# Optimization experiments

Measured on AMD Instinct MI355X. Metric: run time of the kernel, lower is better.

## Reference

```python
import jax, jax.numpy as jnp
import numpy as np

DIM = 512          # model dim
DH = 32            # dim_head
WSZ = 8            # window_size
HEADS = DIM // DH  # 16
INNER = HEADS * DH # 512
D4 = DIM // 4      # DPB hidden = 128
EPS = 1e-5


def _ln(x, g, b=None, eps=EPS):
    m = jnp.mean(x, axis=-1, keepdims=True)
    v = jnp.var(x, axis=-1, keepdims=True)
    y = (x - m) * jax.lax.rsqrt(v + eps) * g
    return y if b is None else y + b


def setup_inputs() -> dict:
    key = jax.random.key(0)
    ks = jax.random.split(key, 8)
    g = lambda k, shape, s=0.02: (jax.random.normal(k, shape, jnp.float32) * s)
    return {
        "x": jax.random.normal(ks[0], (16, 64, 64, DIM), jnp.float32),
        "norm_g": jnp.ones((DIM,), jnp.float32),
        "norm_b": jnp.zeros((DIM,), jnp.float32),
        "w_qkv": g(ks[1], (DIM, 3 * INNER)),
        "w_out": g(ks[2], (INNER, DIM)),
        "b_out": jnp.zeros((DIM,), jnp.float32),
        "dpb_w0": g(ks[3], (2, D4)), "dpb_b0": jnp.zeros((D4,), jnp.float32), "dpb_ln0": jnp.ones((D4,), jnp.float32),
        "dpb_w1": g(ks[4], (D4, D4)), "dpb_b1": jnp.zeros((D4,), jnp.float32), "dpb_ln1": jnp.ones((D4,), jnp.float32),
        "dpb_w2": g(ks[5], (D4, D4)), "dpb_b2": jnp.zeros((D4,), jnp.float32), "dpb_ln2": jnp.ones((D4,), jnp.float32),
        "dpb_w3": g(ks[6], (D4, 1)), "dpb_b3": jnp.zeros((1,), jnp.float32),
    }


def reference(x, norm_g, norm_b, w_qkv, w_out, b_out,
              dpb_w0, dpb_b0, dpb_ln0,
              dpb_w1, dpb_b1, dpb_ln1,
              dpb_w2, dpb_b2, dpb_ln2,
              dpb_w3, dpb_b3):
    B, H, W, d = x.shape
    w = WSZ
    scale = DH ** -0.5

    x = _ln(x, norm_g, norm_b)

    # 'short' attention: partition into non-overlapping wxw windows
    # b (h s1) (w s2) d -> (b h w) s1 s2 d
    xw = x.reshape(B, H // w, w, W // w, w, d).transpose(0, 1, 3, 2, 4, 5)
    xw = xw.reshape(-1, w, w, d)  # [nb, w, w, d]

    qkv = xw @ w_qkv  # 1x1 conv == dense, no bias
    q, k, v = jnp.split(qkv, 3, axis=-1)
    to_heads = lambda t: t.reshape(t.shape[0], w * w, HEADS, DH).transpose(0, 2, 1, 3)
    q, k, v = map(to_heads, (q, k, v))  # [nb, h, w*w, dh]

    sim = jnp.einsum('bhid,bhjd->bhij', q * scale, k)  # [nb, h, w*w, w*w]

    # relative-position gather indices (static)
    pos = jnp.arange(w)
    grid = jnp.stack(jnp.meshgrid(pos, pos, indexing='ij'), axis=-1).reshape(-1, 2)
    rel = grid[:, None] - grid[None, :] + (w - 1)
    rel_pos_indices = rel[..., 0] * (2 * w - 1) + rel[..., 1]  # [w*w, w*w]

    # dynamic position bias MLP over the (2w+1)^2 relative offsets
    p = jnp.arange(-w, w + 1)
    rp = jnp.stack(jnp.meshgrid(p, p, indexing='ij'), axis=-1).reshape(-1, 2).astype(jnp.float32)
    h = jax.nn.relu(_ln(rp @ dpb_w0 + dpb_b0, dpb_ln0))
    h = jax.nn.relu(_ln(h @ dpb_w1 + dpb_b1, dpb_ln1))
    h = jax.nn.relu(_ln(h @ dpb_w2 + dpb_b2, dpb_ln2))
    biases = (h @ dpb_w3 + dpb_b3)[:, 0]  # [(2w+1)^2]

    sim = sim + biases[rel_pos_indices]
    attn = jax.nn.softmax(sim, axis=-1)
    out = jnp.einsum('bhij,bhjd->bhid', attn, v)

    out = out.transpose(0, 2, 1, 3).reshape(-1, w, w, INNER)
    out = out @ w_out + b_out  # 1x1 conv with bias

    # (b h w) s1 s2 d -> b (h s1) (w s2) d
    out = out.reshape(B, H // w, W // w, w, w, d).transpose(0, 1, 3, 2, 4, 5)
    return out.reshape(B, H, W, d)
```

## Files before the change

### kernel.cpp

```cpp
#include <hip/hip_runtime.h>
#include <cstdint>
#include <cstddef>

typedef unsigned short u16;
typedef __attribute__((ext_vector_type(8))) short short8;
typedef __attribute__((ext_vector_type(4))) float f32x4;
typedef __attribute__((ext_vector_type(4))) unsigned short us4;

#define AS1 __attribute__((address_space(1)))
#define AS3 __attribute__((address_space(3)))

__device__ __forceinline__ u16 f2bf(float f) {
  union { float f; unsigned u; } v; v.f = f;
  unsigned r = v.u + 0x7fffu + ((v.u >> 16) & 1u);
  return (u16)(r >> 16);
}

__device__ __forceinline__ void gload_lds16(const u16* g, u16* l) {
  __builtin_amdgcn_global_load_lds((AS1 void*)g, (AS3 void*)l, 16, 0, 0);
}

__global__ void ln_cast_kernel(const float* __restrict__ x, const float* __restrict__ g,
                               const float* __restrict__ b, u16* __restrict__ out) {
  const int lane = threadIdx.x & 63;
  const int tok = blockIdx.x * 4 + (threadIdx.x >> 6);
  const float4* row = (const float4*)(x + (size_t)tok * 512);
  float4 v0 = row[lane];
  float4 v1 = row[lane + 64];
  float s = v0.x + v0.y + v0.z + v0.w + v1.x + v1.y + v1.z + v1.w;
  float q = v0.x*v0.x + v0.y*v0.y + v0.z*v0.z + v0.w*v0.w
          + v1.x*v1.x + v1.y*v1.y + v1.z*v1.z + v1.w*v1.w;
#pragma unroll
  for (int m = 1; m < 64; m <<= 1) { s += __shfl_xor(s, m, 64); q += __shfl_xor(q, m, 64); }
  const float mean = s * (1.0f / 512.0f);
  const float var = q * (1.0f / 512.0f) - mean * mean;
  const float r = rsqrtf(var + 1e-5f);
  const float4* g4 = (const float4*)g;
  const float4* b4 = (const float4*)b;
  float4 ga = g4[lane], gb = g4[lane + 64];
  float4 ba = b4[lane], bb = b4[lane + 64];
  us4 o0 = { f2bf((v0.x - mean) * r * ga.x + ba.x), f2bf((v0.y - mean) * r * ga.y + ba.y),
             f2bf((v0.z - mean) * r * ga.z + ba.z), f2bf((v0.w - mean) * r * ga.w + ba.w) };
  us4 o1 = { f2bf((v1.x - mean) * r * gb.x + bb.x), f2bf((v1.y - mean) * r * gb.y + bb.y),
             f2bf((v1.z - mean) * r * gb.z + bb.z), f2bf((v1.w - mean) * r * gb.w + bb.w) };
  *(us4*)(out + (size_t)tok * 512 + lane * 4) = o0;
  *(us4*)(out + (size_t)tok * 512 + 256 + lane * 4) = o1;
}

__global__ void prep_w_kernel(const float* __restrict__ wqkv, const float* __restrict__ wout,
                              u16* __restrict__ wqkvT, u16* __restrict__ woutT) {
  int idx = blockIdx.x * blockDim.x + threadIdx.x;
  if (idx < 512 * 1536) {
    int n = idx >> 9, k = idx & 511;
    wqkvT[idx] = f2bf(wqkv[k * 1536 + n]);
  } else {
    int j = idx - 512 * 1536;
    if (j < 512 * 512) {
      int n = j >> 9, k = j & 511;
      woutT[j] = f2bf(wout[k * 512 + n]);
    }
  }
}

__device__ __forceinline__ float lnrelu128(float a, float g, float* red, int tid) {
  float s = a, q = a * a;
#pragma unroll
  for (int m = 1; m < 64; m <<= 1) { s += __shfl_xor(s, m, 64); q += __shfl_xor(q, m, 64); }
  __syncthreads();
  if ((tid & 63) == 0) { red[tid >> 6] = s; red[2 + (tid >> 6)] = q; }
  __syncthreads();
  float S = red[0] + red[1], Q = red[2] + red[3];
  float mean = S * (1.f / 128.f);
  float var = Q * (1.f / 128.f) - mean * mean;
  float y = (a - mean) * rsqrtf(var + 1e-5f) * g;
  return fmaxf(y, 0.f);
}

__global__ void dpb_mlp_kernel(const float* __restrict__ w0, const float* __restrict__ b0, const float* __restrict__ g0,
                               const float* __restrict__ w1, const float* __restrict__ b1, const float* __restrict__ g1,
                               const float* __restrict__ w2, const float* __restrict__ b2, const float* __restrict__ g2,
                               const float* __restrict__ w3, const float* __restrict__ b3,
                               float* __restrict__ biases) {
  __shared__ float h[128];
  __shared__ float red[4];
  const int tid = threadIdx.x;
  const int row = blockIdx.x;
  const float p0 = (float)(row / 17) - 8.0f;
  const float p1 = (float)(row % 17) - 8.0f;
  float a = p0 * w0[tid] + p1 * w0[128 + tid] + b0[tid];
  a = lnrelu128(a, g0[tid], red, tid);
  h[tid] = a;
  __syncthreads();
  float acc = b1[tid];
  for (int i = 0; i < 128; ++i) acc += h[i] * w1[i * 128 + tid];
  acc = lnrelu128(acc, g1[tid], red, tid);
  h[tid] = acc;
  __syncthreads();
  float acc2 = b2[tid];
  for (int i = 0; i < 128; ++i) acc2 += h[i] * w2[i * 128 + tid];
  acc2 = lnrelu128(acc2, g2[tid], red, tid);
  float t = acc2 * w3[tid];
#pragma unroll
  for (int m = 1; m < 64; m <<= 1) t += __shfl_xor(t, m, 64);
  __syncthreads();
  if ((tid & 63) == 0) red[tid >> 6] = t;
  __syncthreads();
  if (tid == 0) biases[row] = red[0] + red[1] + b3[0];
}

__global__ void dpb_table_kernel(const float* __restrict__ biases, float* __restrict__ table) {
  int t = blockIdx.x * blockDim.x + threadIdx.x;
  if (t < 4096) {
    int i = t >> 6, j = t & 63;
    int r0 = (i >> 3) - (j >> 3) + 7;
    int r1 = (i & 7) - (j & 7) + 7;
    table[t] = biases[r0 * 15 + r1];
  }
}

template <int CT, bool F32OUT>
__global__ __launch_bounds__(512, 2) void gemm256_kernel(const u16* __restrict__ A, const u16* __restrict__ BT,
                                                         void* __restrict__ Cv, const float* __restrict__ bias) {
  __shared__ __align__(16) u16 lds[65536];
  const int tid = threadIdx.x;
  const int w = tid >> 6, l = tid & 63;
  const int wm = w >> 2, wn = w & 3;
  const int cr = l & 15, cg = l >> 4;
  const int pc8 = (cg ^ ((cr + (cr >> 2)) & 3)) * 8;

  const int hw = blockIdx.x;
  const int ix = hw >> 3;
  const int rt = (hw & 7) + 8 * (ix / CT);
  const int ct = ix % CT;
  const size_t brow = (size_t)rt * 256;
  const size_t bcol = (size_t)ct * 256;
  const int N = CT * 256;

  const int srow = tid >> 2;
  const int sch8 = ((tid & 3) ^ ((srow + (srow >> 2)) & 3)) * 8;

  const f32x4 zero = {0.f, 0.f, 0.f, 0.f};
  f32x4 acc[8][4];
#pragma unroll
  for (int i = 0; i < 8; ++i)
#pragma unroll
    for (int j = 0; j < 4; ++j) acc[i][j] = zero;

  const u16* aP = &lds[(wm * 128 + cr) * 32 + pc8];
  const u16* bP = &lds[(wn * 64 + cr) * 32 + pc8];

#define STAGE_HALF(G, GROW0, KCOL, LBASE)                                          \
  do {                                                                             \
    const u16* g0_ = (G) + ((GROW0) + srow) * 512 + (KCOL) + sch8;                 \
    gload_lds16(g0_, &lds[(LBASE) + w * 512]);                                     \
    gload_lds16(g0_ + 128 * 512, &lds[(LBASE) + 4096 + w * 512]);                  \
  } while (0)

  STAGE_HALF(A, brow, 0, 0);
  STAGE_HALF(BT, bcol, 0, 32768);
  STAGE_HALF(A, brow, 32, 8192);
  STAGE_HALF(BT, bcol, 32, 32768 + 8192);
  asm volatile("s_waitcnt vmcnt(4)" ::: "memory");
  __builtin_amdgcn_s_barrier();
  __builtin_amdgcn_sched_barrier(0);

#pragma unroll 2
  for (int kt = 0; kt < 8; ++kt) {
    const int cur = kt & 1;
    const int nbuf = cur ^ 1;
    const int ktn = (kt < 7) ? kt + 1 : 7;
    const int kcn = ktn * 64;
    const int abase = cur * 16384;
    const int bbase = 32768 + cur * 16384;
    short8 af[8], bfr[4];

#pragma unroll
    for (int fr = 0; fr < 8; ++fr) af[fr] = *(const short8*)(aP + abase + fr * 512);
#pragma unroll
    for (int c = 0; c < 4; ++c) bfr[c] = *(const short8*)(bP + bbase + c * 512);
    STAGE_HALF(A, brow, kcn, nbuf * 16384);
    STAGE_HALF(BT, bcol, kcn, 32768 + nbuf * 16384);
    asm volatile("s_waitcnt lgkmcnt(0)" ::: "memory");
    __builtin_amdgcn_sched_barrier(0);
    __builtin_amdgcn_s_setprio(1);
#pragma unroll
    for (int fr = 0; fr < 8; ++fr)
#pragma unroll
      for (int fc = 0; fc < 4; ++fc)
        acc[fr][fc] = __builtin_amdgcn_mfma_f32_16x16x32_bf16(bfr[fc], af[fr], acc[fr][fc], 0, 0, 0);
    __builtin_amdgcn_s_setprio(0);
    asm volatile("s_waitcnt vmcnt(4)" ::: "memory");
    __builtin_amdgcn_s_barrier();
    __builtin_amdgcn_sched_barrier(0);

#pragma unroll
    for (int fr = 0; fr < 8; ++fr) af[fr] = *(const short8*)(aP + abase + 8192 + fr * 512);
#pragma unroll
    for (int c = 0; c < 4; ++c) bfr[c] = *(const short8*)(bP + bbase + 8192 + c * 512);
    STAGE_HALF(A, brow, kcn + 32, nbuf * 16384 + 8192);
    STAGE_HALF(BT, bcol, kcn + 32, 32768 + nbuf * 16384 + 8192);
    asm volatile("s_waitcnt lgkmcnt(0)" ::: "memory");
    __builtin_amdgcn_sched_barrier(0);
    __builtin_amdgcn_s_setprio(1);
#pragma unroll
    for (int fr = 0; fr < 8; ++fr)
#pragma unroll
      for (int fc = 0; fc < 4; ++fc)
        acc[fr][fc] = __builtin_amdgcn_mfma_f32_16x16x32_bf16(bfr[fc], af[fr], acc[fr][fc], 0, 0, 0);
    __builtin_amdgcn_s_setprio(0);
    asm volatile("s_waitcnt vmcnt(4)" ::: "memory");
    __builtin_amdgcn_s_barrier();
    __builtin_amdgcn_sched_barrier(0);
  }
#undef STAGE_HALF

  asm volatile("s_waitcnt vmcnt(0)" ::: "memory");
  __builtin_amdgcn_sched_barrier(0);

  if (F32OUT) {
    float* C = (float*)Cv;
#pragma unroll
    for (int fc = 0; fc < 4; ++fc) {
      size_t col = bcol + wn * 64 + fc * 16 + cg * 4;
      float4 bv = *(const float4*)&bias[col];
#pragma unroll
      for (int fr = 0; fr < 8; ++fr) {
        size_t r = brow + wm * 128 + fr * 16 + cr;
        float4 o = { acc[fr][fc][0] + bv.x, acc[fr][fc][1] + bv.y,
                     acc[fr][fc][2] + bv.z, acc[fr][fc][3] + bv.w };
        *(float4*)(C + r * N + col) = o;
      }
    }
  } else {
    u16* C = (u16*)Cv;
#pragma unroll
    for (int fc = 0; fc < 4; ++fc) {
      size_t col = bcol + wn * 64 + fc * 16 + cg * 4;
#pragma unroll
      for (int fr = 0; fr < 8; ++fr) {
        size_t r = brow + wm * 128 + fr * 16 + cr;
        uint2 p;
        p.x = (unsigned)f2bf(acc[fr][fc][0]) | ((unsigned)f2bf(acc[fr][fc][1]) << 16);
        p.y = (unsigned)f2bf(acc[fr][fc][2]) | ((unsigned)f2bf(acc[fr][fc][3]) << 16);
        *(uint2*)(C + r * N + col) = p;
      }
    }
  }
}

__global__ __launch_bounds__(64) void attn_kernel(const u16* __restrict__ qkv,
                                                  const float* __restrict__ table,
                                                  u16* __restrict__ aout) {
  __shared__ __align__(16) u16 P[64 * 72];
  __shared__ __align__(16) u16 VT[32 * 72];
  const int l = threadIdx.x;
  const int cr = l & 15, cg = l >> 4;
  const int head = blockIdx.x & 15;
  const int win = blockIdx.x >> 4;
  const int base = ((win >> 6) << 12) + (((win >> 3) & 7) << 9) + ((win & 7) << 3);

  {
    const size_t row = base + ((l >> 3) << 6) + (l & 7);
    const u16* vp = qkv + row * 1536 + 1024 + head * 32;
    short8 v0 = *(const short8*)(vp);
    short8 v1 = *(const short8*)(vp + 8);
    short8 v2 = *(const short8*)(vp + 16);
    short8 v3 = *(const short8*)(vp + 24);
#pragma unroll
    for (int j = 0; j < 8; ++j) {
      VT[j * 72 + l] = (u16)v0[j];
      VT[(8 + j) * 72 + l] = (u16)v1[j];
      VT[(16 + j) * 72 + l] = (u16)v2[j];
      VT[(24 + j) * 72 + l] = (u16)v3[j];
    }
  }

  short8 qf[4], kf[4];
#pragma unroll
  for (int mt = 0; mt < 4; ++mt) {
    int t = mt * 16 + cr;
    size_t row = base + ((t >> 3) << 6) + (t & 7);
    qf[mt] = *(const short8*)(qkv + row * 1536 + head * 32 + cg * 8);
    kf[mt] = *(const short8*)(qkv + row * 1536 + 512 + head * 32 + cg * 8);
  }

  const f32x4 zero = {0.f, 0.f, 0.f, 0.f};
  f32x4 s[4][4];
#pragma unroll
  for (int mt = 0; mt < 4; ++mt)
#pragma unroll
    for (int nt = 0; nt < 4; ++nt)
      s[mt][nt] = __builtin_amdgcn_mfma_f32_16x16x32_bf16(qf[mt], kf[nt], zero, 0, 0, 0);

  const float scale = 0.17677669529663689f;
#pragma unroll
  for (int mt = 0; mt < 4; ++mt) {
#pragma unroll
    for (int reg = 0; reg < 4; ++reg) {
      const int r = mt * 16 + cg * 4 + reg;
      float v[4];
      float mx = -3.0e38f;
#pragma unroll
      for (int nt = 0; nt < 4; ++nt) {
        v[nt] = s[mt][nt][reg] * scale + table[r * 64 + nt * 16 + cr];
        mx = fmaxf(mx, v[nt]);
      }
#pragma unroll
      for (int m2 = 1; m2 < 16; m2 <<= 1) mx = fmaxf(mx, __shfl_xor(mx, m2, 64));
      float sum = 0.f;
#pragma unroll
      for (int nt = 0; nt < 4; ++nt) { v[nt] = __expf(v[nt] - mx); sum += v[nt]; }
#pragma unroll
      for (int m2 = 1; m2 < 16; m2 <<= 1) sum += __shfl_xor(sum, m2, 64);
      float inv = 1.0f / sum;
#pragma unroll
      for (int nt = 0; nt < 4; ++nt) P[r * 72 + nt * 16 + cr] = f2bf(v[nt] * inv);
    }
  }
  __syncthreads();

  f32x4 o[4][2];
#pragma unroll
  for (int mt = 0; mt < 4; ++mt) { o[mt][0] = zero; o[mt][1] = zero; }
#pragma unroll
  for (int kk = 0; kk < 2; ++kk) {
    short8 pf[4], vf[2];
#pragma unroll
    for (int mt = 0; mt < 4; ++mt) pf[mt] = *(const short8*)&P[(mt * 16 + cr) * 72 + kk * 32 + cg * 8];
#pragma unroll
    for (int n2 = 0; n2 < 2; ++n2) vf[n2] = *(const short8*)&VT[(n2 * 16 + cr) * 72 + kk * 32 + cg * 8];
#pragma unroll
    for (int mt = 0; mt < 4; ++mt)
#pragma unroll
      for (int n2 = 0; n2 < 2; ++n2)
        o[mt][n2] = __builtin_amdgcn_mfma_f32_16x16x32_bf16(pf[mt], vf[n2], o[mt][n2], 0, 0, 0);
  }

#pragma unroll
  for (int mt = 0; mt < 4; ++mt)
#pragma unroll
    for (int n2 = 0; n2 < 2; ++n2)
#pragma unroll
      for (int reg = 0; reg < 4; ++reg) {
        int t = mt * 16 + cg * 4 + reg;
        size_t row = base + ((t >> 3) << 6) + (t & 7);
        aout[row * 512 + head * 32 + n2 * 16 + cr] = f2bf(o[mt][n2][reg]);
      }
}

extern "C" void kernel_launch(void* const* d_in, const int* in_sizes, int n_in,
                              void* d_out, int out_size, void* d_ws, size_t ws_size,
                              hipStream_t stream) {
  const float* x = (const float*)d_in[0];
  const float* norm_g = (const float*)d_in[1];
  const float* norm_b = (const float*)d_in[2];
  const float* w_qkv = (const float*)d_in[3];
  const float* w_out = (const float*)d_in[4];
  const float* b_out = (const float*)d_in[5];
  const float* dw0 = (const float*)d_in[6];
  const float* db0 = (const float*)d_in[7];
  const float* dg0 = (const float*)d_in[8];
  const float* dw1 = (const float*)d_in[9];
  const float* db1 = (const float*)d_in[10];
  const float* dg1 = (const float*)d_in[11];
  const float* dw2 = (const float*)d_in[12];
  const float* db2 = (const float*)d_in[13];
  const float* dg2 = (const float*)d_in[14];
  const float* dw3 = (const float*)d_in[15];
  const float* db3 = (const float*)d_in[16];

  char* ws = (char*)d_ws;
  size_t off = 0;
  auto take = [&](size_t bytes) { char* p = ws + off; off += (bytes + 255) & ~(size_t)255; return p; };
  u16* xln = (u16*)take(65536ull * 512 * 2);
  u16* wqkvT = (u16*)take(1536 * 512 * 2);
  u16* woutT = (u16*)take(512 * 512 * 2);
  float* biases = (float*)take(289 * 4);
  float* table = (float*)take(4096 * 4);

  size_t rem = (ws_size > off) ? ws_size - off : 0;
  int nch = 4;
  if (rem >= 65536ull * 2048 * 2 + 512) nch = 1;
  else if (rem >= 32768ull * 2048 * 2 + 512) nch = 2;
  const int rows = 65536 / nch;
  u16* qkvbuf = (u16*)take((size_t)rows * 1536 * 2);
  u16* attnbuf = (u16*)take((size_t)rows * 512 * 2);

  ln_cast_kernel<<<16384, 256, 0, stream>>>(x, norm_g, norm_b, xln);
  prep_w_kernel<<<4096, 256, 0, stream>>>(w_qkv, w_out, wqkvT, woutT);
  dpb_mlp_kernel<<<289, 128, 0, stream>>>(dw0, db0, dg0, dw1, db1, dg1, dw2, db2, dg2, dw3, db3, biases);
  dpb_table_kernel<<<16, 256, 0, stream>>>(biases, table);

  for (int c = 0; c < nch; ++c) {
    const u16* Ac = xln + (size_t)c * rows * 512;
    gemm256_kernel<6, false><<<(rows / 256) * 6, 512, 0, stream>>>(Ac, wqkvT, (void*)qkvbuf, nullptr);
    attn_kernel<<<(rows / 64) * 16, 64, 0, stream>>>(qkvbuf, table, attnbuf);
    float* Cc = (float*)d_out + (size_t)c * rows * 512;
    gemm256_kernel<2, true><<<(rows / 256) * 2, 512, 0, stream>>>(attnbuf, woutT, (void*)Cc, b_out);
  }
}
```

Baseline: 388.8 us.

## Replace 256x256 double-buffered GEMM with simpler 128x128 single-buffered tile GEMM

Swaps the 256x256-tile GEMM, which used 512 threads, double-buffered LDS staging and hand-placed waitcnt/priority scheduling, for a 128x128-tile kernel with 256 threads and a single LDS buffer. The new kernel does one synchronized load-then-compute step per 32-wide K slice. Smaller tiles give more blocks and higher occupancy (launch bounds 256,4). The cost is less data reuse per tile and no overlap of global loads with MFMA work, since each K step waits on a barrier after its loads.

```diff
diff --git a/kernel.cpp b/kernel.cpp
--- a/kernel.cpp
+++ b/kernel.cpp
@@ -119,12 +119,13 @@
 }
 
 template <int CT, bool F32OUT>
-__global__ __launch_bounds__(512, 2) void gemm256_kernel(const u16* __restrict__ A, const u16* __restrict__ BT,
+__global__ __launch_bounds__(256, 4) void gemm128_kernel(const u16* __restrict__ A, const u16* __restrict__ BT,
                                                          void* __restrict__ Cv, const float* __restrict__ bias) {
-  __shared__ __align__(16) u16 lds[65536];
+  __shared__ __align__(16) u16 As[128 * 32];
+  __shared__ __align__(16) u16 Bs[128 * 32];
   const int tid = threadIdx.x;
   const int w = tid >> 6, l = tid & 63;
-  const int wm = w >> 2, wn = w & 3;
+  const int wr = w >> 1, wc = w & 1;
   const int cr = l & 15, cg = l >> 4;
   const int pc8 = (cg ^ ((cr + (cr >> 2)) & 3)) * 8;
 
@@ -132,100 +133,53 @@
   const int ix = hw >> 3;
   const int rt = (hw & 7) + 8 * (ix / CT);
   const int ct = ix % CT;
-  const size_t brow = (size_t)rt * 256;
-  const size_t bcol = (size_t)ct * 256;
-  const int N = CT * 256;
+  const size_t brow = (size_t)rt * 128;
+  const size_t bcol = (size_t)ct * 128;
+  const int N = CT * 128;
 
   const int srow = tid >> 2;
-  const int sch8 = ((tid & 3) ^ ((srow + (srow >> 2)) & 3)) * 8;
+  const int csrc8 = ((tid & 3) ^ ((srow + (srow >> 2)) & 3)) * 8;
+  const u16* gA = A + (brow + srow) * 512 + csrc8;
+  const u16* gB = BT + (bcol + srow) * 512 + csrc8;
 
   const f32x4 zero = {0.f, 0.f, 0.f, 0.f};
-  f32x4 acc[8][4];
-#pragma unroll
-  for (int i = 0; i < 8; ++i)
+  f32x4 acc[4][4];
+#pragma unroll
+  for (int i = 0; i < 4; ++i)
 #pragma unroll
     for (int j = 0; j < 4; ++j) acc[i][j] = zero;
 
-  const u16* aP = &lds[(wm * 128 + cr) * 32 + pc8];
-  const u16* bP = &lds[(wn * 64 + cr) * 32 + pc8];
-
-#define STAGE_HALF(G, GROW0, KCOL, LBASE)                                          \
-  do {                                                                             \
-    const u16* g0_ = (G) + ((GROW0) + srow) * 512 + (KCOL) + sch8;                 \
-    gload_lds16(g0_, &lds[(LBASE) + w * 512]);                                     \
-    gload_lds16(g0_ + 128 * 512, &lds[(LBASE) + 4096 + w * 512]);                  \
-  } while (0)
-
-  STAGE_HALF(A, brow, 0, 0);
-  STAGE_HALF(BT, bcol, 0, 32768);
-  STAGE_HALF(A, brow, 32, 8192);
-  STAGE_HALF(BT, bcol, 32, 32768 + 8192);
-  asm volatile("s_waitcnt vmcnt(4)" ::: "memory");
-  __builtin_amdgcn_s_barrier();
-  __builtin_amdgcn_sched_barrier(0);
-
-#pragma unroll 2
-  for (int kt = 0; kt < 8; ++kt) {
-    const int cur = kt & 1;
-    const int nbuf = cur ^ 1;
-    const int ktn = (kt < 7) ? kt + 1 : 7;
-    const int kcn = ktn * 64;
-    const int abase = cur * 16384;
-    const int bbase = 32768 + cur * 16384;
-    short8 af[8], bfr[4];
-
-#pragma unroll
-    for (int fr = 0; fr < 8; ++fr) af[fr] = *(const short8*)(aP + abase + fr * 512);
-#pragma unroll
-    for (int c = 0; c < 4; ++c) bfr[c] = *(const short8*)(bP + bbase + c * 512);
-    STAGE_HALF(A, brow, kcn, nbuf * 16384);
-    STAGE_HALF(BT, bcol, kcn, 32768 + nbuf * 16384);
-    asm volatile("s_waitcnt lgkmcnt(0)" ::: "memory");
-    __builtin_amdgcn_sched_barrier(0);
-    __builtin_amdgcn_s_setprio(1);
-#pragma unroll
-    for (int fr = 0; fr < 8; ++fr)
+  const u16* aP = &As[(wr * 64 + cr) * 32 + pc8];
+  const u16* bP = &Bs[(wc * 64 + cr) * 32 + pc8];
+
+  for (int k0 = 0; k0 < 512; k0 += 32) {
+    gload_lds16(gA + k0, &As[w * 512]);
+    gload_lds16(gA + k0 + 64 * 512, &As[2048 + w * 512]);
+    gload_lds16(gB + k0, &Bs[w * 512]);
+    gload_lds16(gB + k0 + 64 * 512, &Bs[2048 + w * 512]);
+    __syncthreads();
+    short8 af[4], bf[4];
+#pragma unroll
+    for (int fr = 0; fr < 4; ++fr) af[fr] = *(const short8*)(aP + fr * 512);
+#pragma unroll
+    for (int fc = 0; fc < 4; ++fc) bf[fc] = *(const short8*)(bP + fc * 512);
+#pragma unroll
+    for (int fr = 0; fr < 4; ++fr)
 #pragma unroll
       for (int fc = 0; fc < 4; ++fc)
-        acc[fr][fc] = __builtin_amdgcn_mfma_f32_16x16x32_bf16(bfr[fc], af[fr], acc[fr][fc], 0, 0, 0);
-    __builtin_amdgcn_s_setprio(0);
-    asm volatile("s_waitcnt vmcnt(4)" ::: "memory");
-    __builtin_amdgcn_s_barrier();
-    __builtin_amdgcn_sched_barrier(0);
-
-#pragma unroll
-    for (int fr = 0; fr < 8; ++fr) af[fr] = *(const short8*)(aP + abase + 8192 + fr * 512);
-#pragma unroll
-    for (int c = 0; c < 4; ++c) bfr[c] = *(const short8*)(bP + bbase + 8192 + c * 512);
-    STAGE_HALF(A, brow, kcn + 32, nbuf * 16384 + 8192);
-    STAGE_HALF(BT, bcol, kcn + 32, 32768 + nbuf * 16384 + 8192);
-    asm volatile("s_waitcnt lgkmcnt(0)" ::: "memory");
-    __builtin_amdgcn_sched_barrier(0);
-    __builtin_amdgcn_s_setprio(1);
-#pragma unroll
-    for (int fr = 0; fr < 8; ++fr)
-#pragma unroll
-      for (int fc = 0; fc < 4; ++fc)
-        acc[fr][fc] = __builtin_amdgcn_mfma_f32_16x16x32_bf16(bfr[fc], af[fr], acc[fr][fc], 0, 0, 0);
-    __builtin_amdgcn_s_setprio(0);
-    asm volatile("s_waitcnt vmcnt(4)" ::: "memory");
-    __builtin_amdgcn_s_barrier();
-    __builtin_amdgcn_sched_barrier(0);
-  }
-#undef STAGE_HALF
-
-  asm volatile("s_waitcnt vmcnt(0)" ::: "memory");
-  __builtin_amdgcn_sched_barrier(0);
+        acc[fr][fc] = __builtin_amdgcn_mfma_f32_16x16x32_bf16(bf[fc], af[fr], acc[fr][fc], 0, 0, 0);
+    __syncthreads();
+  }
 
   if (F32OUT) {
     float* C = (float*)Cv;
 #pragma unroll
     for (int fc = 0; fc < 4; ++fc) {
-      size_t col = bcol + wn * 64 + fc * 16 + cg * 4;
+      size_t col = bcol + wc * 64 + fc * 16 + cg * 4;
       float4 bv = *(const float4*)&bias[col];
 #pragma unroll
-      for (int fr = 0; fr < 8; ++fr) {
-        size_t r = brow + wm * 128 + fr * 16 + cr;
+      for (int fr = 0; fr < 4; ++fr) {
+        size_t r = brow + wr * 64 + fr * 16 + cr;
         float4 o = { acc[fr][fc][0] + bv.x, acc[fr][fc][1] + bv.y,
                      acc[fr][fc][2] + bv.z, acc[fr][fc][3] + bv.w };
         *(float4*)(C + r * N + col) = o;
@@ -235,10 +189,10 @@
     u16* C = (u16*)Cv;
 #pragma unroll
     for (int fc = 0; fc < 4; ++fc) {
-      size_t col = bcol + wn * 64 + fc * 16 + cg * 4;
-#pragma unroll
-      for (int fr = 0; fr < 8; ++fr) {
-        size_t r = brow + wm * 128 + fr * 16 + cr;
+      size_t col = bcol + wc * 64 + fc * 16 + cg * 4;
+#pragma unroll
+      for (int fr = 0; fr < 4; ++fr) {
+        size_t r = brow + wr * 64 + fr * 16 + cr;
         uint2 p;
         p.x = (unsigned)f2bf(acc[fr][fc][0]) | ((unsigned)f2bf(acc[fr][fc][1]) << 16);
         p.y = (unsigned)f2bf(acc[fr][fc][2]) | ((unsigned)f2bf(acc[fr][fc][3]) << 16);
@@ -393,9 +347,9 @@
 
   for (int c = 0; c < nch; ++c) {
     const u16* Ac = xln + (size_t)c * rows * 512;
-    gemm256_kernel<6, false><<<(rows / 256) * 6, 512, 0, stream>>>(Ac, wqkvT, (void*)qkvbuf, nullptr);
+    gemm128_kernel<12, false><<<(rows / 128) * 12, 256, 0, stream>>>(Ac, wqkvT, (void*)qkvbuf, nullptr);
     attn_kernel<<<(rows / 64) * 16, 64, 0, stream>>>(qkvbuf, table, attnbuf);
     float* Cc = (float*)d_out + (size_t)c * rows * 512;
-    gemm256_kernel<2, true><<<(rows / 256) * 2, 512, 0, stream>>>(attnbuf, woutT, (void*)Cc, b_out);
-  }
-}
+    gemm128_kernel<4, true><<<(rows / 128) * 4, 256, 0, stream>>>(attnbuf, woutT, (void*)Cc, b_out);
+  }
+}
```

After: 384.4 us. No clear change (-1.1%).
